# Performance work log

Measured on AMD Instinct MI355X. Metric: run time of the kernel, lower is better.

Reference implementation:

```python
import jax, jax.numpy as jnp
import numpy as np

HIDDEN = 2048
NH = 32          # num attention heads
NKV = 8          # num key/value heads
HD = HIDDEN // NH  # head_dim = 64
ROPE_BASE = 10000.0
NEG_INF = -1e9


def _rope_interleaved(t, positions):
    # t: [b, s, h, d], interleaved RoPE over full head_dim (flash-attn RotaryEmbedding(interleaved=True))
    d = t.shape[-1]
    inv_freq = 1.0 / (ROPE_BASE ** (jnp.arange(0, d, 2, dtype=jnp.float32) / d))
    ang = positions[:, None].astype(jnp.float32) * inv_freq[None, :]  # [s, d/2]
    cos = jnp.cos(ang)[None, :, None, :]
    sin = jnp.sin(ang)[None, :, None, :]
    t1 = t[..., 0::2]
    t2 = t[..., 1::2]
    out_even = t1 * cos - t2 * sin
    out_odd = t1 * sin + t2 * cos
    return jnp.stack([out_even, out_odd], axis=-1).reshape(t.shape)


def setup_inputs() -> dict:
    key = jax.random.key(0)
    k1, k2, k3 = jax.random.split(key, 3)
    B, S = 2, 2048
    x = jax.random.normal(k1, (B, S, HIDDEN), dtype=jnp.float32)
    mask = jnp.ones((B, S), dtype=jnp.int32)  # padding mask, all valid
    total_head_dim = (NH + 2 * NKV) * HD  # 3072
    scale = 1.0 / np.sqrt(HIDDEN)
    w_qkv = jax.random.normal(k2, (HIDDEN, total_head_dim), dtype=jnp.float32) * scale
    w_o = jax.random.normal(k3, (NH * HD, HIDDEN), dtype=jnp.float32) * scale
    return {"x": x, "mask": mask, "w_qkv": w_qkv, "w_o": w_o}


def reference(x, mask, w_qkv, w_o):
    B, S, _ = x.shape
    kv_size = NKV * HD
    qkv = jnp.einsum('bsh,hd->bsd', x, w_qkv)
    q = qkv[..., :HIDDEN].reshape(B, S, NH, HD)
    kv = qkv[..., HIDDEN:].reshape(B, S, 2, NKV, HD)
    pos = jnp.arange(S)  # seqlen_offset = 0 (input_pos None)
    q = _rope_interleaved(q, pos)
    k = _rope_interleaved(kv[:, :, 0], pos)
    v = kv[:, :, 1]
    # GQA: expand kv heads to NH
    groups = NH // NKV
    k = jnp.repeat(k, groups, axis=2)  # [b, s, NH, HD]
    v = jnp.repeat(v, groups, axis=2)
    scores = jnp.einsum('bqhd,bkhd->bhqk', q, k) / np.sqrt(HD)
    causal = jnp.tril(jnp.ones((S, S), dtype=bool))
    key_valid = mask[:, None, None, :] > 0  # [b,1,1,k]
    scores = jnp.where(causal[None, None] & key_valid, scores, NEG_INF)
    probs = jax.nn.softmax(scores, axis=-1)
    attn = jnp.einsum('bhqk,bkhd->bqhd', probs, v)
    # pad_input writes zeros at padded query positions
    attn = attn * (mask[:, :, None, None] > 0)
    attn = attn.reshape(B, S, NH * HD)
    return jnp.einsum('bsd,dh->bsh', attn, w_o)
```

## Files before the change

### kernel.cpp

```cpp
#include <hip/hip_runtime.h>
#include <hip/hip_bf16.h>
#include <cstdint>
#include <cstddef>

typedef __attribute__((ext_vector_type(8))) short bf16x8;
typedef __attribute__((ext_vector_type(4))) float f32x4;

static constexpr int CB  = 2;
static constexpr int CS  = 2048;
static constexpr int CH  = 2048;
static constexpr int CNH = 32;
static constexpr int CNKV = 8;
static constexpr int CHD = 64;
static constexpr int CTHD = 3072;

__device__ __forceinline__ void gload_lds16(const void* g, void* l) {
  __builtin_amdgcn_global_load_lds(
      (const __attribute__((address_space(1))) unsigned int*)g,
      (__attribute__((address_space(3))) unsigned int*)l, 16, 0, 0);
}

__device__ __forceinline__ unsigned short bfbits(float f) {
  __hip_bfloat16 h = __float2bfloat16(f);
  return *(unsigned short*)&h;
}

__global__ void conv_bf16(const float* __restrict__ in, __hip_bfloat16* __restrict__ out, int n) {
  const int i = (blockIdx.x * 256 + threadIdx.x) * 4;
  if (i >= n) return;
  const float4 v = *(const float4*)(in + i);
  out[i]     = __float2bfloat16(v.x);
  out[i + 1] = __float2bfloat16(v.y);
  out[i + 2] = __float2bfloat16(v.z);
  out[i + 3] = __float2bfloat16(v.w);
}

__global__ __launch_bounds__(256) void transpose_conv(const float* __restrict__ in,
                                                      __hip_bfloat16* __restrict__ out,
                                                      int R, int Cc) {
  __shared__ float t[32][33];
  const int nbx = Cc >> 5;
  const int bx = blockIdx.x % nbx, by = blockIdx.x / nbx;
  const int c0 = bx << 5, r0 = by << 5;
  const int tx = threadIdx.x & 31, ty = threadIdx.x >> 5;
#pragma unroll
  for (int j = 0; j < 32; j += 8)
    t[ty + j][tx] = in[(size_t)(r0 + ty + j) * Cc + c0 + tx];
  __syncthreads();
#pragma unroll
  for (int j = 0; j < 32; j += 8)
    out[(size_t)(c0 + ty + j) * R + r0 + tx] = __float2bfloat16(t[tx][ty + j]);
}

template <typename OutT>
__global__ __launch_bounds__(256) void gemm_bt(const __hip_bfloat16* __restrict__ A,
                                               const __hip_bfloat16* __restrict__ Bt,
                                               OutT* __restrict__ C, int M, int N, int K) {
  __shared__ __hip_bfloat16 As[128 * 32];
  __shared__ __hip_bfloat16 Bs[128 * 32];
  const int tid = threadIdx.x;
  const int lane = tid & 63;
  const int wave = tid >> 6;
  const int nTn = N >> 7;
  const int nwg = gridDim.x;
  const int wg = (blockIdx.x & 7) * (nwg >> 3) + (blockIdx.x >> 3);
  const int tm = wg / nTn, tn = wg % nTn;
  const size_t m0 = (size_t)tm * 128, n0 = (size_t)tn * 128;
  const __hip_bfloat16* Ag = A + m0 * K;
  const __hip_bfloat16* Bg = Bt + n0 * K;
  const int wr = wave >> 1, wc = wave & 1;
  const int rsel = lane & 15, k8 = (lane >> 4) << 3;

  f32x4 acc[4][4];
#pragma unroll
  for (int m = 0; m < 4; ++m)
#pragma unroll
    for (int n = 0; n < 4; ++n) acc[m][n] = (f32x4){0.f, 0.f, 0.f, 0.f};

  for (int k0 = 0; k0 < K; k0 += 32) {
    __syncthreads();
#pragma unroll
    for (int i = 0; i < 2; ++i) {
      const int c = i * 256 + tid;
      const int r = c >> 2, kq = (c & 3) << 3;
      gload_lds16(Ag + (size_t)r * K + k0 + kq, &As[(i * 256 + wave * 64) * 8]);
      gload_lds16(Bg + (size_t)r * K + k0 + kq, &Bs[(i * 256 + wave * 64) * 8]);
    }
    __syncthreads();
    bf16x8 af[4], bfr[4];
#pragma unroll
    for (int m = 0; m < 4; ++m)
      af[m] = *(const bf16x8*)&As[(wr * 64 + m * 16 + rsel) * 32 + k8];
#pragma unroll
    for (int n = 0; n < 4; ++n)
      bfr[n] = *(const bf16x8*)&Bs[(wc * 64 + n * 16 + rsel) * 32 + k8];
#pragma unroll
    for (int m = 0; m < 4; ++m)
#pragma unroll
      for (int n = 0; n < 4; ++n)
        acc[m][n] = __builtin_amdgcn_mfma_f32_16x16x32_bf16(af[m], bfr[n], acc[m][n], 0, 0, 0);
  }

  const int rowb = (lane >> 4) << 2;
#pragma unroll
  for (int m = 0; m < 4; ++m)
#pragma unroll
    for (int n = 0; n < 4; ++n) {
      const size_t r0 = m0 + wr * 64 + m * 16 + rowb;
      const size_t cc = n0 + wc * 64 + n * 16 + rsel;
#pragma unroll
      for (int j = 0; j < 4; ++j) {
        const float v = acc[m][n][j];
        if constexpr (sizeof(OutT) == 4)
          C[(r0 + j) * N + cc] = v;
        else
          C[(r0 + j) * N + cc] = __float2bfloat16(v);
      }
    }
}

__global__ void rope_extract(const __hip_bfloat16* __restrict__ qkv,
                             __hip_bfloat16* __restrict__ Q,
                             __hip_bfloat16* __restrict__ Kr) {
  const int idx = blockIdx.x * 256 + threadIdx.x;
  const int i = idx & 31;
  const int hs = (idx >> 5) % 40;
  const int r = idx / (40 * 32);
  const int srow = r & (CS - 1);
  const int b = r >> 11;
  const float inv = exp2f(-(float)i * (13.287712379549449f / 32.0f));
  const float ang = (float)srow * inv;
  const float sn = sinf(ang), cs = cosf(ang);
  const int col = (hs < CNH) ? hs * CHD + 2 * i : CH + (hs - CNH) * CHD + 2 * i;
  const float t1 = __bfloat162float(qkv[(size_t)r * CTHD + col]);
  const float t2 = __bfloat162float(qkv[(size_t)r * CTHD + col + 1]);
  const float ev = t1 * cs - t2 * sn;
  const float ov = t1 * sn + t2 * cs;
  __hip_bfloat16* dst;
  if (hs < CNH)
    dst = Q + ((((size_t)b * CNH + hs) * CS + srow) * CHD + 2 * i);
  else
    dst = Kr + ((((size_t)b * CNKV + (hs - CNH)) * CS + srow) * CHD + 2 * i);
  dst[0] = __float2bfloat16(ev);
  dst[1] = __float2bfloat16(ov);
}

__global__ __launch_bounds__(256) void v_transpose(const __hip_bfloat16* __restrict__ qkv,
                                                   __hip_bfloat16* __restrict__ VT) {
  __shared__ __hip_bfloat16 t[64][72];
  const int bi = blockIdx.x;
  const int stile = bi & 31;
  const int kvh = (bi >> 5) & 7;
  const int b = bi >> 8;
  const int tx = threadIdx.x & 63;
  const int ty = threadIdx.x >> 6;
  const int s0 = stile * 64;
#pragma unroll
  for (int j = 0; j < 16; ++j) {
    const int sl = ty * 16 + j;
    t[sl][tx] = qkv[(size_t)(b * CS + s0 + sl) * CTHD + (CH + CNKV * CHD) + kvh * CHD + tx];
  }
  __syncthreads();
#pragma unroll
  for (int j = 0; j < 16; ++j) {
    const int dl = ty * 16 + j;
    VT[(((size_t)b * CNKV + kvh) * CHD + dl) * CS + s0 + tx] = t[tx][dl];
  }
}

__global__ __launch_bounds__(256) void attn_fa(const __hip_bfloat16* __restrict__ Q,
                                               const __hip_bfloat16* __restrict__ Kr,
                                               const __hip_bfloat16* __restrict__ VT,
                                               const int* __restrict__ mask,
                                               __hip_bfloat16* __restrict__ O) {
  __shared__ __hip_bfloat16 Ks[2][64 * 64];
  __shared__ __hip_bfloat16 Vs[2][64 * 64];
  __shared__ __hip_bfloat16 P4[4][16][72];
  const int kvh = blockIdx.x & 7;
  const int slot = blockIdx.x >> 3;
  const int qw = 127 - (slot >> 1);
  const int b = slot & 1;
  const int tid = threadIdx.x;
  const int wave = tid >> 6, lane = tid & 63;
  const int h = kvh * 4 + wave;
  const int q0 = qw * 16;
  const int rsel = lane & 15;
  const int hi = lane >> 4;
  const int k8 = hi * 8;
  const int rowb = hi * 4;
  const int qr = q0 + rsel;
  const __hip_bfloat16* Qp = Q + (((size_t)b * CNH + h) * CS + q0) * CHD;
  const __hip_bfloat16* Kp = Kr + ((size_t)b * CNKV + kvh) * CS * CHD;
  const __hip_bfloat16* Vp = VT + ((size_t)b * CNKV + kvh) * CHD * CS;
  const int* mp = mask + b * CS;
  __hip_bfloat16(*P)[72] = P4[wave];

  bf16x8 qf[2];
  qf[0] = *(const bf16x8*)(Qp + rsel * CHD + k8);
  qf[1] = *(const bf16x8*)(Qp + rsel * CHD + 32 + k8);

  f32x4 o[4];
#pragma unroll
  for (int nt = 0; nt < 4; ++nt) o[nt] = (f32x4){0.f, 0.f, 0.f, 0.f};
  float mrun = -3e38f, lrun = 0.f;

  const int nkb = (qw >> 2) + 1;

  auto stage = [&](int buf, int key0) {
#pragma unroll
    for (int half = 0; half < 2; ++half) {
      const int c = half * 256 + tid;
      const int r = c >> 3;
      const int swz = ((c & 7) ^ (r & 7)) * 8;
      __hip_bfloat16* kd = &Ks[buf][(half * 256 + wave * 64) * 8];
      __hip_bfloat16* vd = &Vs[buf][(half * 256 + wave * 64) * 8];
      gload_lds16(Kp + (size_t)(key0 + r) * CHD + swz, kd);
      gload_lds16(Vp + (size_t)r * CS + key0 + swz, vd);
    }
  };

  int mcur = mp[lane], mnext = 0;
  stage(0, 0);
  __syncthreads();

  for (int t = 0; t < nkb; ++t) {
    const int cur = t & 1;
    const int key0 = t * 64;
    const bool last = (t == nkb - 1);
    if (!last) {
      stage(cur ^ 1, key0 + 64);
      mnext = mp[key0 + 64 + lane];
    }
    const unsigned long long kvbits = __ballot(mcur > 0);
    const int sz = rsel & 7;
    bf16x8 kc[8];
#pragma unroll
    for (int kt = 0; kt < 4; ++kt) {
      const int row = (kt * 16 + rsel) * 64;
      kc[kt * 2]     = *(const bf16x8*)&Ks[cur][row + ((hi ^ sz) << 3)];
      kc[kt * 2 + 1] = *(const bf16x8*)&Ks[cur][row + (((hi ^ 4) ^ sz) << 3)];
    }
    f32x4 st[4];
#pragma unroll
    for (int kt = 0; kt < 4; ++kt) {
      f32x4 s = (f32x4){0.f, 0.f, 0.f, 0.f};
      s = __builtin_amdgcn_mfma_f32_16x16x32_bf16(kc[kt * 2], qf[0], s, 0, 0, 0);
      s = __builtin_amdgcn_mfma_f32_16x16x32_bf16(kc[kt * 2 + 1], qf[1], s, 0, 0, 0);
      st[kt] = s;
    }
    bf16x8 vf[8];
#pragma unroll
    for (int nt = 0; nt < 4; ++nt) {
      const int row = (nt * 16 + rsel) * 64;
      vf[nt * 2]     = *(const bf16x8*)&Vs[cur][row + ((hi ^ sz) << 3)];
      vf[nt * 2 + 1] = *(const bf16x8*)&Vs[cur][row + (((hi ^ 4) ^ sz) << 3)];
    }
    if (kvbits == ~0ull && !last) {
#pragma unroll
      for (int kt = 0; kt < 4; ++kt)
#pragma unroll
        for (int j = 0; j < 4; ++j) st[kt][j] *= 0.125f;
    } else {
#pragma unroll
      for (int kt = 0; kt < 4; ++kt)
#pragma unroll
        for (int j = 0; j < 4; ++j) {
          const int idx = kt * 16 + rowb + j;
          const bool bad = !((kvbits >> idx) & 1ull) || (last && key0 + idx > qr);
          st[kt][j] = bad ? -1e9f : st[kt][j] * 0.125f;
        }
    }
    float pmax = st[0][0];
#pragma unroll
    for (int kt = 0; kt < 4; ++kt)
#pragma unroll
      for (int j = 0; j < 4; ++j) pmax = fmaxf(pmax, st[kt][j]);
    pmax = fmaxf(pmax, __shfl_xor(pmax, 16));
    pmax = fmaxf(pmax, __shfl_xor(pmax, 32));
    const float mn = fmaxf(mrun, pmax);
    const float al = exp2f((mrun - mn) * 1.44269504f);
    mrun = mn;
    float ps = 0.f;
#pragma unroll
    for (int kt = 0; kt < 4; ++kt)
#pragma unroll
      for (int j = 0; j < 4; ++j) {
        const float p = exp2f((st[kt][j] - mn) * 1.44269504f);
        st[kt][j] = p;
        ps += p;
      }
    ps += __shfl_xor(ps, 16);
    ps += __shfl_xor(ps, 32);
    lrun = lrun * al + ps;
#pragma unroll
    for (int nt = 0; nt < 4; ++nt)
#pragma unroll
      for (int j = 0; j < 4; ++j) o[nt][j] *= al;
#pragma unroll
    for (int kt = 0; kt < 4; ++kt) {
      ushort4 pk;
      pk.x = bfbits(st[kt][0]);
      pk.y = bfbits(st[kt][1]);
      pk.z = bfbits(st[kt][2]);
      pk.w = bfbits(st[kt][3]);
      *(ushort4*)&P[rsel][kt * 16 + rowb] = pk;
    }
    const bf16x8 pb0 = *(const bf16x8*)&P[rsel][k8];
    const bf16x8 pb1 = *(const bf16x8*)&P[rsel][32 + k8];
#pragma unroll
    for (int nt = 0; nt < 4; ++nt) {
      o[nt] = __builtin_amdgcn_mfma_f32_16x16x32_bf16(vf[nt * 2], pb0, o[nt], 0, 0, 0);
      o[nt] = __builtin_amdgcn_mfma_f32_16x16x32_bf16(vf[nt * 2 + 1], pb1, o[nt], 0, 0, 0);
    }
    __syncthreads();
    mcur = mnext;
  }

  const float qm = (mp[qr] > 0) ? 1.0f : 0.0f;
  const float inv = qm / fmaxf(lrun, 1e-20f);
  __hip_bfloat16* Orow = O + (((size_t)b * CS + qr) * CNH + h) * CHD;
#pragma unroll
  for (int nt = 0; nt < 4; ++nt) {
    ushort4 ok;
    ok.x = bfbits(o[nt][0] * inv);
    ok.y = bfbits(o[nt][1] * inv);
    ok.z = bfbits(o[nt][2] * inv);
    ok.w = bfbits(o[nt][3] * inv);
    *(ushort4*)(Orow + nt * 16 + rowb) = ok;
  }
}

extern "C" void kernel_launch(void* const* d_in, const int* in_sizes, int n_in,
                              void* d_out, int out_size, void* d_ws, size_t ws_size,
                              hipStream_t stream) {
  const float* x = (const float*)d_in[0];
  const int* mask = (const int*)d_in[1];
  const float* w_qkv = (const float*)d_in[2];
  const float* w_o = (const float*)d_in[3];
  float* out = (float*)d_out;

  char* ws = (char*)d_ws;
  size_t off = 0;
  auto alloc = [&](size_t bytes) {
    char* p = ws + off;
    off += (bytes + 255) & ~(size_t)255;
    return p;
  };
  const size_t M = (size_t)CB * CS;
  __hip_bfloat16* x_bf  = (__hip_bfloat16*)alloc(M * CH * 2);
  __hip_bfloat16* wqkvT = (__hip_bfloat16*)alloc((size_t)CTHD * CH * 2);
  __hip_bfloat16* woT   = (__hip_bfloat16*)alloc((size_t)CH * CH * 2);
  __hip_bfloat16* qkv   = (__hip_bfloat16*)alloc(M * CTHD * 2);
  __hip_bfloat16* Qb    = (__hip_bfloat16*)alloc((size_t)CB * CNH * CS * CHD * 2);
  __hip_bfloat16* Kb    = (__hip_bfloat16*)alloc((size_t)CB * CNKV * CS * CHD * 2);
  __hip_bfloat16* VTb   = (__hip_bfloat16*)alloc((size_t)CB * CNKV * CHD * CS * 2);
  __hip_bfloat16* attnb = (__hip_bfloat16*)alloc(M * CH * 2);

  conv_bf16<<<(int)(M * CH / 4 / 256), 256, 0, stream>>>(x, x_bf, (int)(M * CH));
  transpose_conv<<<(CTHD / 32) * (CH / 32), 256, 0, stream>>>(w_qkv, wqkvT, CH, CTHD);
  transpose_conv<<<(CH / 32) * (CH / 32), 256, 0, stream>>>(w_o, woT, CH, CH);
  gemm_bt<__hip_bfloat16><<<(int)(M / 128) * (CTHD / 128), 256, 0, stream>>>(
      x_bf, wqkvT, qkv, (int)M, CTHD, CH);
  rope_extract<<<(int)(M * 40 * 32 / 256), 256, 0, stream>>>(qkv, Qb, Kb);
  v_transpose<<<CB * CNKV * 32, 256, 0, stream>>>(qkv, VTb);
  attn_fa<<<CB * CNKV * 128, 256, 0, stream>>>(Qb, Kb, VTb, mask, attnb);
  gemm_bt<float><<<(int)(M / 128) * (CH / 128), 256, 0, stream>>>(
      attnb, woT, out, (int)M, CH, CH);
}
```

Before: 265.6 us.

## Fold softmax scale into Q RoPE, lazy rescale, shuffle P instead of LDS

The softmax scale and log2(e) are folded into Q during RoPE extraction, which removes the per-score multiply and the exp2 argument scaling. The running-max rescale of O and l is skipped unless some lane's block max exceeds the running max by more than 8 (in log2 units). P is now redistributed through cross-lane shuffles rather than an LDS round trip, which frees the P4 shared buffer. The cost is 16 shuffles per tile, a bf16 rounding of the pre-scaled Q, and probabilities that can grow up to 2^8 before a rescale.

```diff
diff --git a/kernel.cpp b/kernel.cpp
--- a/kernel.cpp
+++ b/kernel.cpp
@@ -134,8 +134,9 @@
   const int col = (hs < CNH) ? hs * CHD + 2 * i : CH + (hs - CNH) * CHD + 2 * i;
   const float t1 = __bfloat162float(qkv[(size_t)r * CTHD + col]);
   const float t2 = __bfloat162float(qkv[(size_t)r * CTHD + col + 1]);
-  const float ev = t1 * cs - t2 * sn;
-  const float ov = t1 * sn + t2 * cs;
+  const float scl = (hs < CNH) ? 0.18033688011112042f : 1.0f;
+  const float ev = (t1 * cs - t2 * sn) * scl;
+  const float ov = (t1 * sn + t2 * cs) * scl;
   __hip_bfloat16* dst;
   if (hs < CNH)
     dst = Q + ((((size_t)b * CNH + hs) * CS + srow) * CHD + 2 * i);
@@ -175,7 +176,6 @@
                                                __hip_bfloat16* __restrict__ O) {
   __shared__ __hip_bfloat16 Ks[2][64 * 64];
   __shared__ __hip_bfloat16 Vs[2][64 * 64];
-  __shared__ __hip_bfloat16 P4[4][16][72];
   const int kvh = blockIdx.x & 7;
   const int slot = blockIdx.x >> 3;
   const int qw = 127 - (slot >> 1);
@@ -193,7 +193,6 @@
   const __hip_bfloat16* Kp = Kr + ((size_t)b * CNKV + kvh) * CS * CHD;
   const __hip_bfloat16* Vp = VT + ((size_t)b * CNKV + kvh) * CHD * CS;
   const int* mp = mask + b * CS;
-  __hip_bfloat16(*P)[72] = P4[wave];
 
   bf16x8 qf[2];
   qf[0] = *(const bf16x8*)(Qp + rsel * CHD + k8);
@@ -219,6 +218,10 @@
     }
   };
 
+  const int srcA = rsel + ((hi & 1) << 5);
+  const int srcB = srcA + 16;
+  const bool lowkt = hi < 2;
+
   int mcur = mp[lane], mnext = 0;
   stage(0, 0);
   __syncthreads();
@@ -255,19 +258,14 @@
       vf[nt * 2]     = *(const bf16x8*)&Vs[cur][row + ((hi ^ sz) << 3)];
       vf[nt * 2 + 1] = *(const bf16x8*)&Vs[cur][row + (((hi ^ 4) ^ sz) << 3)];
     }
-    if (kvbits == ~0ull && !last) {
-#pragma unroll
-      for (int kt = 0; kt < 4; ++kt)
-#pragma unroll
-        for (int j = 0; j < 4; ++j) st[kt][j] *= 0.125f;
-    } else {
+    if (!(kvbits == ~0ull && !last)) {
 #pragma unroll
       for (int kt = 0; kt < 4; ++kt)
 #pragma unroll
         for (int j = 0; j < 4; ++j) {
           const int idx = kt * 16 + rowb + j;
           const bool bad = !((kvbits >> idx) & 1ull) || (last && key0 + idx > qr);
-          st[kt][j] = bad ? -1e9f : st[kt][j] * 0.125f;
+          if (bad) st[kt][j] = -1e9f;
         }
     }
     float pmax = st[0][0];
@@ -277,36 +275,64 @@
       for (int j = 0; j < 4; ++j) pmax = fmaxf(pmax, st[kt][j]);
     pmax = fmaxf(pmax, __shfl_xor(pmax, 16));
     pmax = fmaxf(pmax, __shfl_xor(pmax, 32));
-    const float mn = fmaxf(mrun, pmax);
-    const float al = exp2f((mrun - mn) * 1.44269504f);
-    mrun = mn;
+    if (__any(pmax > mrun + 8.0f)) {
+      const float mn = fmaxf(mrun, pmax);
+      const float al = exp2f(mrun - mn);
+      mrun = mn;
+      lrun *= al;
+#pragma unroll
+      for (int nt = 0; nt < 4; ++nt)
+#pragma unroll
+        for (int j = 0; j < 4; ++j) o[nt][j] *= al;
+    }
     float ps = 0.f;
 #pragma unroll
     for (int kt = 0; kt < 4; ++kt)
 #pragma unroll
       for (int j = 0; j < 4; ++j) {
-        const float p = exp2f((st[kt][j] - mn) * 1.44269504f);
+        const float p = exp2f(st[kt][j] - mrun);
         st[kt][j] = p;
         ps += p;
       }
     ps += __shfl_xor(ps, 16);
     ps += __shfl_xor(ps, 32);
-    lrun = lrun * al + ps;
-#pragma unroll
-    for (int nt = 0; nt < 4; ++nt)
-#pragma unroll
-      for (int j = 0; j < 4; ++j) o[nt][j] *= al;
+    lrun += ps;
+    unsigned wv[4][2];
 #pragma unroll
     for (int kt = 0; kt < 4; ++kt) {
-      ushort4 pk;
-      pk.x = bfbits(st[kt][0]);
-      pk.y = bfbits(st[kt][1]);
-      pk.z = bfbits(st[kt][2]);
-      pk.w = bfbits(st[kt][3]);
-      *(ushort4*)&P[rsel][kt * 16 + rowb] = pk;
-    }
-    const bf16x8 pb0 = *(const bf16x8*)&P[rsel][k8];
-    const bf16x8 pb1 = *(const bf16x8*)&P[rsel][32 + k8];
+      wv[kt][0] = (unsigned)bfbits(st[kt][0]) | ((unsigned)bfbits(st[kt][1]) << 16);
+      wv[kt][1] = (unsigned)bfbits(st[kt][2]) | ((unsigned)bfbits(st[kt][3]) << 16);
+    }
+    const unsigned q00A = (unsigned)__shfl((int)wv[0][0], srcA);
+    const unsigned q01A = (unsigned)__shfl((int)wv[0][1], srcA);
+    const unsigned q10A = (unsigned)__shfl((int)wv[1][0], srcA);
+    const unsigned q11A = (unsigned)__shfl((int)wv[1][1], srcA);
+    const unsigned q00B = (unsigned)__shfl((int)wv[0][0], srcB);
+    const unsigned q01B = (unsigned)__shfl((int)wv[0][1], srcB);
+    const unsigned q10B = (unsigned)__shfl((int)wv[1][0], srcB);
+    const unsigned q11B = (unsigned)__shfl((int)wv[1][1], srcB);
+    const unsigned r20A = (unsigned)__shfl((int)wv[2][0], srcA);
+    const unsigned r21A = (unsigned)__shfl((int)wv[2][1], srcA);
+    const unsigned r30A = (unsigned)__shfl((int)wv[3][0], srcA);
+    const unsigned r31A = (unsigned)__shfl((int)wv[3][1], srcA);
+    const unsigned r20B = (unsigned)__shfl((int)wv[2][0], srcB);
+    const unsigned r21B = (unsigned)__shfl((int)wv[2][1], srcB);
+    const unsigned r30B = (unsigned)__shfl((int)wv[3][0], srcB);
+    const unsigned r31B = (unsigned)__shfl((int)wv[3][1], srcB);
+    union {
+      unsigned u[4];
+      bf16x8 v;
+    } ua, ub;
+    ua.u[0] = lowkt ? q00A : q10A;
+    ua.u[1] = lowkt ? q01A : q11A;
+    ua.u[2] = lowkt ? q00B : q10B;
+    ua.u[3] = lowkt ? q01B : q11B;
+    ub.u[0] = lowkt ? r20A : r30A;
+    ub.u[1] = lowkt ? r21A : r31A;
+    ub.u[2] = lowkt ? r20B : r30B;
+    ub.u[3] = lowkt ? r21B : r31B;
+    const bf16x8 pb0 = ua.v;
+    const bf16x8 pb1 = ub.v;
 #pragma unroll
     for (int nt = 0; nt < 4; ++nt) {
       o[nt] = __builtin_amdgcn_mfma_f32_16x16x32_bf16(vf[nt * 2], pb0, o[nt], 0, 0, 0);
```

Result: slower. 272.9 us (+2.8%).
